# Optimization experiments

Measured on AMD Instinct MI355X. Metric: run time of the kernel, lower is better.

The kernel has to match this reference:

```python
import jax, jax.numpy as jnp
import numpy as np

SIGMA = 1.0
RADIUS = int(4.0 * SIGMA + 0.5)  # scipy/skimage truncate=4.0

_t = np.arange(-RADIUS, RADIUS + 1, dtype=np.float32)
_w = np.exp(-0.5 * (_t / SIGMA) ** 2)
KERNEL = jnp.asarray(_w / _w.sum())  # [2*RADIUS+1]


def _blur_axis(x, axis):
    """1D Gaussian filter along `axis` with 'nearest' (edge) boundary."""
    pads = [(0, 0)] * x.ndim
    pads[axis] = (RADIUS, RADIUS)
    xp = jnp.pad(x, pads, mode='edge')
    n = x.shape[axis]
    out = KERNEL[0] * jax.lax.slice_in_dim(xp, 0, n, axis=axis)
    for k in range(1, 2 * RADIUS + 1):
        out = out + KERNEL[k] * jax.lax.slice_in_dim(xp, k, k + n, axis=axis)
    return out


def gaussian_blur(x):
    # skimage.filters.gaussian on each [T, F] sample: blur over both axes
    x = _blur_axis(x, axis=1)  # time axis
    x = _blur_axis(x, axis=2)  # feature axis
    return x


def lstm_last_hidden(x, W_ih, W_hh, b_ih, b_hh):
    B, T, F = x.shape
    H = W_hh.shape[1]
    # precompute input projections for all timesteps: [B, T, 4H]
    xg = jnp.einsum('btf,gf->btg', x, W_ih) + b_ih + b_hh
    xg = jnp.transpose(xg, (1, 0, 2))  # [T, B, 4H]

    def step(carry, xt):
        h, c = carry
        g = xt + h @ W_hh.T  # [B, 4H]
        i, f, gg, o = jnp.split(g, 4, axis=-1)  # torch gate order i,f,g,o
        i = jax.nn.sigmoid(i)
        f = jax.nn.sigmoid(f)
        gg = jnp.tanh(gg)
        o = jax.nn.sigmoid(o)
        c = f * c + i * gg
        h = o * jnp.tanh(c)
        return (h, c), None

    h0 = jnp.zeros((B, H), dtype=x.dtype)
    c0 = jnp.zeros((B, H), dtype=x.dtype)
    (h_last, _), _ = jax.lax.scan(step, (h0, c0), xg)
    return h_last  # [B, H]


def setup_inputs() -> dict:
    key = jax.random.key(0)
    ks = jax.random.split(key, 7)
    B, T, F, H, O = 64, 1024, 256, 1024, 256
    s_ih = 1.0 / np.sqrt(F)
    s_hh = 1.0 / np.sqrt(H)
    return {
        'x': jax.random.uniform(ks[0], (B, T, F), dtype=jnp.float32),
        'W_ih': jax.random.normal(ks[1], (4 * H, F), dtype=jnp.float32) * s_ih,
        'W_hh': jax.random.normal(ks[2], (4 * H, H), dtype=jnp.float32) * s_hh,
        'b_ih': jax.random.normal(ks[3], (4 * H,), dtype=jnp.float32) * s_hh,
        'b_hh': jax.random.normal(ks[4], (4 * H,), dtype=jnp.float32) * s_hh,
        'W_fc': jax.random.normal(ks[5], (O, H), dtype=jnp.float32) * s_hh,
        'b_fc': jax.random.normal(ks[6], (O,), dtype=jnp.float32) * s_hh,
    }


def reference(x, W_ih, W_hh, b_ih, b_hh, W_fc, b_fc):
    xb = gaussian_blur(x)
    h_last = lstm_last_hidden(xb, W_ih, W_hh, b_ih, b_hh)
    return h_last @ W_fc.T + b_fc  # [B, O]
```

## Files before the change

kernel.cpp:

```cpp
#include <hip/hip_runtime.h>

typedef __bf16 bf16x8 __attribute__((ext_vector_type(8)));
typedef float f32x4 __attribute__((ext_vector_type(4)));

#define T_STEPS 1024
#define H_SZ    1024
#define F_IN    256
#define NGROUP  4
#define NB      16
#define WPG     64

__device__ __forceinline__ unsigned short f2bf(float f) {
    union { float f; unsigned u; } v; v.f = f;
    unsigned r = v.u + 0x7fffu + ((v.u >> 16) & 1u);
    return (unsigned short)(r >> 16);
}

__device__ __forceinline__ float fsigmoid(float x) {
    return 1.0f / (1.0f + __expf(-x));
}
__device__ __forceinline__ float ftanh(float x) {
    return 1.0f - 2.0f / (__expf(2.0f * x) + 1.0f);
}

__global__ __launch_bounds__(256) void blur_kernel(
    const float* __restrict__ x, unsigned short* __restrict__ xb)
{
    __shared__ float tb[64][256];
    const float kk[9] = {
        0.000133831f, 0.0044318617f, 0.0539911273f, 0.2419714457f,
        0.3989434694f,
        0.2419714457f, 0.0539911273f, 0.0044318617f, 0.000133831f };

    const int b     = blockIdx.x >> 4;
    const int chunk = blockIdx.x & 15;
    const int t0    = chunk * 64;
    const int f     = threadIdx.x;
    const float* xbase = x + (size_t)b * T_STEPS * F_IN;

    for (int r = 0; r < 64; r++) {
        int t = t0 + r;
        float acc = 0.0f;
        #pragma unroll
        for (int d = 0; d < 9; d++) {
            int ts = t + d - 4;
            ts = min(max(ts, 0), T_STEPS - 1);
            acc += kk[d] * xbase[ts * F_IN + f];
        }
        tb[r][f] = acc;
    }
    __syncthreads();
    for (int r = 0; r < 64; r++) {
        float acc = 0.0f;
        #pragma unroll
        for (int d = 0; d < 9; d++) {
            int fs = f + d - 4;
            fs = min(max(fs, 0), F_IN - 1);
            acc += kk[d] * tb[r][fs];
        }
        xb[((size_t)b * T_STEPS + t0 + r) * F_IN + f] = f2bf(acc);
    }
}

__global__ __launch_bounds__(256, 1) void lstm_persist(
    const unsigned short* __restrict__ xb,
    const float* __restrict__ Whh,
    const float* __restrict__ Wih,
    const float* __restrict__ bih,
    const float* __restrict__ bhh,
    unsigned short* __restrict__ hbuf,
    unsigned int* __restrict__ arrive)
{
    const int wg   = blockIdx.x;
    const int grp  = wg >> 6;
    const int w    = wg & 63;
    const int tid  = threadIdx.x;
    const int q    = tid >> 6;
    const int lane = tid & 63;
    const int lrow = lane & 15;
    const int lq   = lane >> 4;

    __shared__ f32x4 part[4][4][64];

    bf16x8 wa[8][4];
    bf16x8 wx[2][4];
    const int row_lo = w * 16 + lrow;
    #pragma unroll
    for (int kt = 0; kt < 8; kt++) {
        const int kofs = q * 256 + kt * 32 + lq * 8;
        #pragma unroll
        for (int g = 0; g < 4; g++) {
            const float* src = Whh + (size_t)(g * H_SZ + row_lo) * H_SZ + kofs;
            union { bf16x8 v; unsigned short s[8]; } u;
            #pragma unroll
            for (int j = 0; j < 8; j++) u.s[j] = f2bf(src[j]);
            wa[kt][g] = u.v;
        }
    }
    #pragma unroll
    for (int kt = 0; kt < 2; kt++) {
        const int kofs = q * 64 + kt * 32 + lq * 8;
        #pragma unroll
        for (int g = 0; g < 4; g++) {
            const float* src = Wih + (size_t)(g * H_SZ + row_lo) * F_IN + kofs;
            union { bf16x8 v; unsigned short s[8]; } u;
            #pragma unroll
            for (int j = 0; j < 8; j++) u.s[j] = f2bf(src[j]);
            wx[kt][g] = u.v;
        }
    }

    const int uhid = tid & 15;
    const int ub   = tid >> 4;
    float bias[4];
    #pragma unroll
    for (int g = 0; g < 4; g++) {
        int r = g * H_SZ + w * 16 + uhid;
        bias[g] = bih[r] + bhh[r];
    }
    float c_reg = 0.0f;

    const int b_abs_l = grp * NB + lrow;
    const unsigned short* xrow_base =
        xb + ((size_t)b_abs_l * T_STEPS) * F_IN + q * 64 + lq * 8;
    unsigned short* hdst =
        hbuf + (size_t)(grp * NB + ub) * H_SZ + w * 16 + uhid;

    for (int t = 0; t < T_STEPS; t++) {
        const unsigned short* xrow = xrow_base + (size_t)t * F_IN;
        bf16x8 xf0 = *reinterpret_cast<const bf16x8*>(xrow);
        bf16x8 xf1 = *reinterpret_cast<const bf16x8*>(xrow + 32);

        const unsigned short* hprev =
            hbuf + ((size_t)((t & 1) ^ 1) * 64 + b_abs_l) * H_SZ
                 + q * 256 + lq * 8;
        bf16x8 hf0, hf1, hf2, hf3, hf4, hf5, hf6, hf7;
        asm volatile(
            "global_load_dwordx4 %0, %8, off sc0 sc1\n\t"
            "global_load_dwordx4 %1, %8, off offset:64 sc0 sc1\n\t"
            "global_load_dwordx4 %2, %8, off offset:128 sc0 sc1\n\t"
            "global_load_dwordx4 %3, %8, off offset:192 sc0 sc1\n\t"
            "global_load_dwordx4 %4, %8, off offset:256 sc0 sc1\n\t"
            "global_load_dwordx4 %5, %8, off offset:320 sc0 sc1\n\t"
            "global_load_dwordx4 %6, %8, off offset:384 sc0 sc1\n\t"
            "global_load_dwordx4 %7, %8, off offset:448 sc0 sc1\n\t"
            "s_waitcnt vmcnt(0)"
            : "=&v"(hf0), "=&v"(hf1), "=&v"(hf2), "=&v"(hf3),
              "=&v"(hf4), "=&v"(hf5), "=&v"(hf6), "=&v"(hf7)
            : "v"(hprev)
            : "memory");
        bf16x8 hfa[8] = { hf0, hf1, hf2, hf3, hf4, hf5, hf6, hf7 };

        f32x4 acc[4];
        #pragma unroll
        for (int g = 0; g < 4; g++) acc[g] = (f32x4){0.f, 0.f, 0.f, 0.f};
        #pragma unroll
        for (int kt = 0; kt < 8; kt++)
            #pragma unroll
            for (int g = 0; g < 4; g++)
                acc[g] = __builtin_amdgcn_mfma_f32_16x16x32_bf16(
                    wa[kt][g], hfa[kt], acc[g], 0, 0, 0);
        acc[0] = __builtin_amdgcn_mfma_f32_16x16x32_bf16(wx[0][0], xf0, acc[0], 0, 0, 0);
        acc[1] = __builtin_amdgcn_mfma_f32_16x16x32_bf16(wx[0][1], xf0, acc[1], 0, 0, 0);
        acc[2] = __builtin_amdgcn_mfma_f32_16x16x32_bf16(wx[0][2], xf0, acc[2], 0, 0, 0);
        acc[3] = __builtin_amdgcn_mfma_f32_16x16x32_bf16(wx[0][3], xf0, acc[3], 0, 0, 0);
        acc[0] = __builtin_amdgcn_mfma_f32_16x16x32_bf16(wx[1][0], xf1, acc[0], 0, 0, 0);
        acc[1] = __builtin_amdgcn_mfma_f32_16x16x32_bf16(wx[1][1], xf1, acc[1], 0, 0, 0);
        acc[2] = __builtin_amdgcn_mfma_f32_16x16x32_bf16(wx[1][2], xf1, acc[2], 0, 0, 0);
        acc[3] = __builtin_amdgcn_mfma_f32_16x16x32_bf16(wx[1][3], xf1, acc[3], 0, 0, 0);

        #pragma unroll
        for (int g = 0; g < 4; g++)
            part[q][g][lane] = acc[g];
        __syncthreads();

        float gv[4];
        #pragma unroll
        for (int g = 0; g < 4; g++) {
            float s = bias[g];
            #pragma unroll
            for (int qq = 0; qq < 4; qq++)
                s += part[qq][g][(uhid >> 2) * 16 + ub][uhid & 3];
            gv[g] = s;
        }
        float ig = fsigmoid(gv[0]);
        float fg = fsigmoid(gv[1]);
        float gg = ftanh(gv[2]);
        float og = fsigmoid(gv[3]);
        c_reg = fg * c_reg + ig * gg;
        float hv = og * ftanh(c_reg);

        unsigned short hb = f2bf(hv);
        unsigned short* dst = hdst + (size_t)(t & 1) * 64 * H_SZ;
        asm volatile(
            "global_store_short %0, %1, off sc0 sc1\n\t"
            "s_waitcnt vmcnt(0)"
            :: "v"(dst), "v"(hb)
            : "memory");
        __syncthreads();

        if (tid == 0) {
            unsigned int* ctr = &arrive[grp * T_STEPS + t];
            __hip_atomic_fetch_add(ctr, 1u, __ATOMIC_RELAXED,
                                   __HIP_MEMORY_SCOPE_AGENT);
            while (__hip_atomic_load(ctr, __ATOMIC_RELAXED,
                                     __HIP_MEMORY_SCOPE_AGENT) < (unsigned)WPG) {}
        }
        __syncthreads();
    }
}

__global__ __launch_bounds__(256) void final_fc(
    const unsigned short* __restrict__ hbuf,
    const float* __restrict__ Wfc, const float* __restrict__ bfc,
    float* __restrict__ out)
{
    __shared__ float hs[H_SZ];
    const int b = blockIdx.x;
    const unsigned short* hrow = hbuf + (size_t)64 * H_SZ + (size_t)b * H_SZ;
    for (int k = threadIdx.x; k < H_SZ; k += 256) {
        union { unsigned u; float f; } cv;
        cv.u = ((unsigned)hrow[k]) << 16;
        hs[k] = cv.f;
    }
    __syncthreads();
    const int o = threadIdx.x;
    const float4* wr = reinterpret_cast<const float4*>(Wfc + (size_t)o * H_SZ);
    float acc = bfc[o];
    for (int k4 = 0; k4 < H_SZ / 4; k4++) {
        float4 wv = wr[k4];
        acc += hs[k4 * 4 + 0] * wv.x + hs[k4 * 4 + 1] * wv.y
             + hs[k4 * 4 + 2] * wv.z + hs[k4 * 4 + 3] * wv.w;
    }
    out[(size_t)b * 256 + o] = acc;
}

extern "C" void kernel_launch(void* const* d_in, const int* in_sizes, int n_in,
                              void* d_out, int out_size, void* d_ws,
                              size_t ws_size, hipStream_t stream)
{
    (void)in_sizes; (void)n_in; (void)out_size; (void)ws_size;
    const float* x   = (const float*)d_in[0];
    const float* Wih = (const float*)d_in[1];
    const float* Whh = (const float*)d_in[2];
    const float* bih = (const float*)d_in[3];
    const float* bhh = (const float*)d_in[4];
    const float* Wfc = (const float*)d_in[5];
    const float* bfc = (const float*)d_in[6];
    float* out = (float*)d_out;

    char* ws = (char*)d_ws;
    unsigned short* xblur = (unsigned short*)ws;
    unsigned short* hbuf  = (unsigned short*)(ws + 33554432);
    unsigned int*   arrv  = (unsigned int*)(ws + 33554432 + 262144);

    hipMemsetAsync(hbuf, 0, 262144 + 16384, stream);

    blur_kernel<<<dim3(1024), dim3(256), 0, stream>>>(x, xblur);

    void* kargs[] = { (void*)&xblur, (void*)&Whh, (void*)&Wih,
                      (void*)&bih, (void*)&bhh, (void*)&hbuf, (void*)&arrv };
    hipLaunchCooperativeKernel((void*)lstm_persist, dim3(256), dim3(256),
                               kargs, 0, stream);

    final_fc<<<dim3(64), dim3(256), 0, stream>>>(hbuf, Wfc, bfc, out);
}
```

Measured before the change: 4.169 ms.

## Replace per-step atomic barrier with timestep-tagged hidden-state words and polling

Each hidden value is now stored as a 32-bit word with the step index in the upper half. Consumers poll their slice of the previous hidden state until every tag matches, then unpack the bf16 halves with perm instructions. This removes the per-step atomic counter, the spin barrier, the store wait and two __syncthreads, and double-buffers the LDS partials so one barrier per step is enough. In exchange it doubles the hidden-state read traffic and polls repeatedly. Correctness now depends on each 32-bit word being stored and loaded as a single unit.

Result: slower. 6.527 ms (+56.5%).

```diff
diff --git a/kernel.cpp b/kernel.cpp
--- a/kernel.cpp
+++ b/kernel.cpp
@@ -2,13 +2,12 @@
 
 typedef __bf16 bf16x8 __attribute__((ext_vector_type(8)));
 typedef float f32x4 __attribute__((ext_vector_type(4)));
+typedef int i32x4 __attribute__((ext_vector_type(4)));
 
 #define T_STEPS 1024
 #define H_SZ    1024
 #define F_IN    256
-#define NGROUP  4
 #define NB      16
-#define WPG     64
 
 __device__ __forceinline__ unsigned short f2bf(float f) {
     union { float f; unsigned u; } v; v.f = f;
@@ -68,8 +67,7 @@
     const float* __restrict__ Wih,
     const float* __restrict__ bih,
     const float* __restrict__ bhh,
-    unsigned short* __restrict__ hbuf,
-    unsigned int* __restrict__ arrive)
+    unsigned int* __restrict__ hbuf)
 {
     const int wg   = blockIdx.x;
     const int grp  = wg >> 6;
@@ -80,7 +78,7 @@
     const int lrow = lane & 15;
     const int lq   = lane >> 4;
 
-    __shared__ f32x4 part[4][4][64];
+    __shared__ f32x4 part[2][4][4][64];
 
     bf16x8 wa[8][4];
     bf16x8 wx[2][4];
@@ -123,7 +121,7 @@
     const int b_abs_l = grp * NB + lrow;
     const unsigned short* xrow_base =
         xb + ((size_t)b_abs_l * T_STEPS) * F_IN + q * 64 + lq * 8;
-    unsigned short* hdst =
+    unsigned int* hdst0 =
         hbuf + (size_t)(grp * NB + ub) * H_SZ + w * 16 + uhid;
 
     for (int t = 0; t < T_STEPS; t++) {
@@ -131,25 +129,65 @@
         bf16x8 xf0 = *reinterpret_cast<const bf16x8*>(xrow);
         bf16x8 xf1 = *reinterpret_cast<const bf16x8*>(xrow + 32);
 
-        const unsigned short* hprev =
-            hbuf + ((size_t)((t & 1) ^ 1) * 64 + b_abs_l) * H_SZ
+        const unsigned int* hprev =
+            hbuf + ((size_t)((t + 1) & 1) * 64 + b_abs_l) * H_SZ
                  + q * 256 + lq * 8;
-        bf16x8 hf0, hf1, hf2, hf3, hf4, hf5, hf6, hf7;
-        asm volatile(
-            "global_load_dwordx4 %0, %8, off sc0 sc1\n\t"
-            "global_load_dwordx4 %1, %8, off offset:64 sc0 sc1\n\t"
-            "global_load_dwordx4 %2, %8, off offset:128 sc0 sc1\n\t"
-            "global_load_dwordx4 %3, %8, off offset:192 sc0 sc1\n\t"
-            "global_load_dwordx4 %4, %8, off offset:256 sc0 sc1\n\t"
-            "global_load_dwordx4 %5, %8, off offset:320 sc0 sc1\n\t"
-            "global_load_dwordx4 %6, %8, off offset:384 sc0 sc1\n\t"
-            "global_load_dwordx4 %7, %8, off offset:448 sc0 sc1\n\t"
-            "s_waitcnt vmcnt(0)"
-            : "=&v"(hf0), "=&v"(hf1), "=&v"(hf2), "=&v"(hf3),
-              "=&v"(hf4), "=&v"(hf5), "=&v"(hf6), "=&v"(hf7)
-            : "v"(hprev)
-            : "memory");
-        bf16x8 hfa[8] = { hf0, hf1, hf2, hf3, hf4, hf5, hf6, hf7 };
+        const unsigned int expect = (unsigned)t;
+        i32x4 d0, d1, d2, d3, d4, d5, d6, d7;
+        i32x4 d8, d9, d10, d11, d12, d13, d14, d15;
+        for (;;) {
+            asm volatile(
+                "global_load_dwordx4 %0,  %16, off sc0 sc1\n\t"
+                "global_load_dwordx4 %1,  %16, off offset:16 sc0 sc1\n\t"
+                "global_load_dwordx4 %2,  %16, off offset:128 sc0 sc1\n\t"
+                "global_load_dwordx4 %3,  %16, off offset:144 sc0 sc1\n\t"
+                "global_load_dwordx4 %4,  %16, off offset:256 sc0 sc1\n\t"
+                "global_load_dwordx4 %5,  %16, off offset:272 sc0 sc1\n\t"
+                "global_load_dwordx4 %6,  %16, off offset:384 sc0 sc1\n\t"
+                "global_load_dwordx4 %7,  %16, off offset:400 sc0 sc1\n\t"
+                "global_load_dwordx4 %8,  %16, off offset:512 sc0 sc1\n\t"
+                "global_load_dwordx4 %9,  %16, off offset:528 sc0 sc1\n\t"
+                "global_load_dwordx4 %10, %16, off offset:640 sc0 sc1\n\t"
+                "global_load_dwordx4 %11, %16, off offset:656 sc0 sc1\n\t"
+                "global_load_dwordx4 %12, %16, off offset:768 sc0 sc1\n\t"
+                "global_load_dwordx4 %13, %16, off offset:784 sc0 sc1\n\t"
+                "global_load_dwordx4 %14, %16, off offset:896 sc0 sc1\n\t"
+                "global_load_dwordx4 %15, %16, off offset:912 sc0 sc1\n\t"
+                "s_waitcnt vmcnt(0)"
+                : "=&v"(d0), "=&v"(d1), "=&v"(d2), "=&v"(d3),
+                  "=&v"(d4), "=&v"(d5), "=&v"(d6), "=&v"(d7),
+                  "=&v"(d8), "=&v"(d9), "=&v"(d10), "=&v"(d11),
+                  "=&v"(d12), "=&v"(d13), "=&v"(d14), "=&v"(d15)
+                : "v"(hprev)
+                : "memory");
+            unsigned bad = 0u;
+            const i32x4* dv[16] = { &d0,&d1,&d2,&d3,&d4,&d5,&d6,&d7,
+                                    &d8,&d9,&d10,&d11,&d12,&d13,&d14,&d15 };
+            #pragma unroll
+            for (int i = 0; i < 16; i++)
+                #pragma unroll
+                for (int j = 0; j < 4; j++)
+                    bad |= (((unsigned)((*dv[i])[j])) >> 16) ^ expect;
+            if (__all((int)(bad == 0u))) break;
+            __builtin_amdgcn_s_sleep(1);
+        }
+
+        bf16x8 hfa[8];
+        {
+            const i32x4* dv[16] = { &d0,&d1,&d2,&d3,&d4,&d5,&d6,&d7,
+                                    &d8,&d9,&d10,&d11,&d12,&d13,&d14,&d15 };
+            #pragma unroll
+            for (int kt = 0; kt < 8; kt++) {
+                const unsigned* a = (const unsigned*)dv[2 * kt];
+                const unsigned* b = (const unsigned*)dv[2 * kt + 1];
+                union { bf16x8 v; unsigned u32[4]; } u;
+                u.u32[0] = __builtin_amdgcn_perm(a[1], a[0], 0x05040100);
+                u.u32[1] = __builtin_amdgcn_perm(a[3], a[2], 0x05040100);
+                u.u32[2] = __builtin_amdgcn_perm(b[1], b[0], 0x05040100);
+                u.u32[3] = __builtin_amdgcn_perm(b[3], b[2], 0x05040100);
+                hfa[kt] = u.v;
+            }
+        }
 
         f32x4 acc[4];
         #pragma unroll
@@ -160,18 +198,18 @@
             for (int g = 0; g < 4; g++)
                 acc[g] = __builtin_amdgcn_mfma_f32_16x16x32_bf16(
                     wa[kt][g], hfa[kt], acc[g], 0, 0, 0);
-        acc[0] = __builtin_amdgcn_mfma_f32_16x16x32_bf16(wx[0][0], xf0, acc[0], 0, 0, 0);
-        acc[1] = __builtin_amdgcn_mfma_f32_16x16x32_bf16(wx[0][1], xf0, acc[1], 0, 0, 0);
-        acc[2] = __builtin_amdgcn_mfma_f32_16x16x32_bf16(wx[0][2], xf0, acc[2], 0, 0, 0);
-        acc[3] = __builtin_amdgcn_mfma_f32_16x16x32_bf16(wx[0][3], xf0, acc[3], 0, 0, 0);
-        acc[0] = __builtin_amdgcn_mfma_f32_16x16x32_bf16(wx[1][0], xf1, acc[0], 0, 0, 0);
-        acc[1] = __builtin_amdgcn_mfma_f32_16x16x32_bf16(wx[1][1], xf1, acc[1], 0, 0, 0);
-        acc[2] = __builtin_amdgcn_mfma_f32_16x16x32_bf16(wx[1][2], xf1, acc[2], 0, 0, 0);
-        acc[3] = __builtin_amdgcn_mfma_f32_16x16x32_bf16(wx[1][3], xf1, acc[3], 0, 0, 0);
-
         #pragma unroll
         for (int g = 0; g < 4; g++)
-            part[q][g][lane] = acc[g];
+            acc[g] = __builtin_amdgcn_mfma_f32_16x16x32_bf16(
+                wx[0][g], xf0, acc[g], 0, 0, 0);
+        #pragma unroll
+        for (int g = 0; g < 4; g++)
+            acc[g] = __builtin_amdgcn_mfma_f32_16x16x32_bf16(
+                wx[1][g], xf1, acc[g], 0, 0, 0);
+
+        #pragma unroll
+        for (int g = 0; g < 4; g++)
+            part[t & 1][q][g][lane] = acc[g];
         __syncthreads();
 
         float gv[4];
@@ -180,7 +218,7 @@
             float s = bias[g];
             #pragma unroll
             for (int qq = 0; qq < 4; qq++)
-                s += part[qq][g][(uhid >> 2) * 16 + ub][uhid & 3];
+                s += part[t & 1][qq][g][(uhid >> 2) * 16 + ub][uhid & 3];
             gv[g] = s;
         }
         float ig = fsigmoid(gv[0]);
@@ -190,38 +228,35 @@
         c_reg = fg * c_reg + ig * gg;
         float hv = og * ftanh(c_reg);
 
-        unsigned short hb = f2bf(hv);
-        unsigned short* dst = hdst + (size_t)(t & 1) * 64 * H_SZ;
-        asm volatile(
-            "global_store_short %0, %1, off sc0 sc1\n\t"
-            "s_waitcnt vmcnt(0)"
-            :: "v"(dst), "v"(hb)
-            : "memory");
-        __syncthreads();
-
-        if (tid == 0) {
-            unsigned int* ctr = &arrive[grp * T_STEPS + t];
-            __hip_atomic_fetch_add(ctr, 1u, __ATOMIC_RELAXED,
-                                   __HIP_MEMORY_SCOPE_AGENT);
-            while (__hip_atomic_load(ctr, __ATOMIC_RELAXED,
-                                     __HIP_MEMORY_SCOPE_AGENT) < (unsigned)WPG) {}
-        }
-        __syncthreads();
-    }
+        unsigned int word = (((unsigned)t + 1u) << 16) | (unsigned)f2bf(hv);
+        unsigned int* dst = hdst0 + (size_t)(t & 1) * 64 * H_SZ;
+        asm volatile("global_store_dword %0, %1, off sc0 sc1"
+                     :: "v"(dst), "v"(word) : "memory");
+    }
+
+    asm volatile("s_waitcnt vmcnt(0)" ::: "memory");
 }
 
 __global__ __launch_bounds__(256) void final_fc(
-    const unsigned short* __restrict__ hbuf,
+    const unsigned int* __restrict__ hbuf,
     const float* __restrict__ Wfc, const float* __restrict__ bfc,
     float* __restrict__ out)
 {
     __shared__ float hs[H_SZ];
     const int b = blockIdx.x;
-    const unsigned short* hrow = hbuf + (size_t)64 * H_SZ + (size_t)b * H_SZ;
-    for (int k = threadIdx.x; k < H_SZ; k += 256) {
-        union { unsigned u; float f; } cv;
-        cv.u = ((unsigned)hrow[k]) << 16;
-        hs[k] = cv.f;
+    const unsigned int* hrow = hbuf + (size_t)64 * H_SZ + (size_t)b * H_SZ;
+    {
+        const unsigned int* src = hrow + threadIdx.x * 4;
+        i32x4 hv4;
+        asm volatile("global_load_dwordx4 %0, %1, off sc0 sc1\n\t"
+                     "s_waitcnt vmcnt(0)"
+                     : "=v"(hv4) : "v"(src) : "memory");
+        #pragma unroll
+        for (int j = 0; j < 4; j++) {
+            union { unsigned u; float f; } cv;
+            cv.u = (((unsigned)hv4[j]) & 0xffffu) << 16;
+            hs[threadIdx.x * 4 + j] = cv.f;
+        }
     }
     __syncthreads();
     const int o = threadIdx.x;
@@ -251,17 +286,21 @@
 
     char* ws = (char*)d_ws;
     unsigned short* xblur = (unsigned short*)ws;
-    unsigned short* hbuf  = (unsigned short*)(ws + 33554432);
-    unsigned int*   arrv  = (unsigned int*)(ws + 33554432 + 262144);
-
-    hipMemsetAsync(hbuf, 0, 262144 + 16384, stream);
+    unsigned int*   hbuf  = (unsigned int*)(ws + 33554432);
+
+    hipMemsetAsync(hbuf, 0, 524288, stream);
 
     blur_kernel<<<dim3(1024), dim3(256), 0, stream>>>(x, xblur);
 
     void* kargs[] = { (void*)&xblur, (void*)&Whh, (void*)&Wih,
-                      (void*)&bih, (void*)&bhh, (void*)&hbuf, (void*)&arrv };
-    hipLaunchCooperativeKernel((void*)lstm_persist, dim3(256), dim3(256),
-                               kargs, 0, stream);
+                      (void*)&bih, (void*)&bhh, (void*)&hbuf };
+    hipError_t ce = hipLaunchCooperativeKernel((void*)lstm_persist, dim3(256),
+                                               dim3(256), kargs, 0, stream);
+    if (ce != hipSuccess) {
+        (void)hipGetLastError();
+        lstm_persist<<<dim3(256), dim3(256), 0, stream>>>(
+            xblur, Whh, Wih, bih, bhh, hbuf);
+    }
 
     final_fc<<<dim3(64), dim3(256), 0, stream>>>(hbuf, Wfc, bfc, out);
 }
```

## Replace per-step atomic counter barrier with per-workgroup step flags polled per wave

Applied to the files above, without the earlier changes.

Each workgroup in the persistent LSTM now publishes its completed step number to its own flag slot. Every wave polls all 64 flags of its group (one per lane) with a wave-wide vote before loading the previous hidden state. This replaces the atomic-increment-and-spin done by one thread, removes a block-wide sync per step, and lets the x loads for the next step be issued before the wait. The final FC kernel also loads hidden values with one vector load per thread, and the launch falls back to a normal kernel launch if the cooperative launch fails. The trade-off is more polling traffic from every wave, and correctness now depends on the double-buffer ordering argument instead of an explicit full barrier.

After: 5.039 ms. +20.9%, slower.

```diff
diff --git a/kernel.cpp b/kernel.cpp
--- a/kernel.cpp
+++ b/kernel.cpp
@@ -2,13 +2,12 @@
 
 typedef __bf16 bf16x8 __attribute__((ext_vector_type(8)));
 typedef float f32x4 __attribute__((ext_vector_type(4)));
+typedef int i32x2 __attribute__((ext_vector_type(2)));
 
 #define T_STEPS 1024
 #define H_SZ    1024
 #define F_IN    256
-#define NGROUP  4
 #define NB      16
-#define WPG     64
 
 __device__ __forceinline__ unsigned short f2bf(float f) {
     union { float f; unsigned u; } v; v.f = f;
@@ -69,7 +68,7 @@
     const float* __restrict__ bih,
     const float* __restrict__ bhh,
     unsigned short* __restrict__ hbuf,
-    unsigned int* __restrict__ arrive)
+    unsigned int* __restrict__ flags)
 {
     const int wg   = blockIdx.x;
     const int grp  = wg >> 6;
@@ -123,16 +122,27 @@
     const int b_abs_l = grp * NB + lrow;
     const unsigned short* xrow_base =
         xb + ((size_t)b_abs_l * T_STEPS) * F_IN + q * 64 + lq * 8;
-    unsigned short* hdst =
+    unsigned short* hdst0 =
         hbuf + (size_t)(grp * NB + ub) * H_SZ + w * 16 + uhid;
+    const unsigned int* flag_rd = flags + ((size_t)grp << 10) + lane;
+    unsigned int* flag_wr = flags + ((size_t)grp << 10) + w;
 
     for (int t = 0; t < T_STEPS; t++) {
         const unsigned short* xrow = xrow_base + (size_t)t * F_IN;
         bf16x8 xf0 = *reinterpret_cast<const bf16x8*>(xrow);
         bf16x8 xf1 = *reinterpret_cast<const bf16x8*>(xrow + 32);
 
+        for (;;) {
+            unsigned fv;
+            asm volatile("global_load_dword %0, %1, off sc0 sc1\n\t"
+                         "s_waitcnt vmcnt(0)"
+                         : "=v"(fv) : "v"(flag_rd) : "memory");
+            if (__all((int)(fv >= (unsigned)t))) break;
+            __builtin_amdgcn_s_sleep(1);
+        }
+
         const unsigned short* hprev =
-            hbuf + ((size_t)((t & 1) ^ 1) * 64 + b_abs_l) * H_SZ
+            hbuf + ((size_t)((t + 1) & 1) * 64 + b_abs_l) * H_SZ
                  + q * 256 + lq * 8;
         bf16x8 hf0, hf1, hf2, hf3, hf4, hf5, hf6, hf7;
         asm volatile(
@@ -160,14 +170,14 @@
             for (int g = 0; g < 4; g++)
                 acc[g] = __builtin_amdgcn_mfma_f32_16x16x32_bf16(
                     wa[kt][g], hfa[kt], acc[g], 0, 0, 0);
-        acc[0] = __builtin_amdgcn_mfma_f32_16x16x32_bf16(wx[0][0], xf0, acc[0], 0, 0, 0);
-        acc[1] = __builtin_amdgcn_mfma_f32_16x16x32_bf16(wx[0][1], xf0, acc[1], 0, 0, 0);
-        acc[2] = __builtin_amdgcn_mfma_f32_16x16x32_bf16(wx[0][2], xf0, acc[2], 0, 0, 0);
-        acc[3] = __builtin_amdgcn_mfma_f32_16x16x32_bf16(wx[0][3], xf0, acc[3], 0, 0, 0);
-        acc[0] = __builtin_amdgcn_mfma_f32_16x16x32_bf16(wx[1][0], xf1, acc[0], 0, 0, 0);
-        acc[1] = __builtin_amdgcn_mfma_f32_16x16x32_bf16(wx[1][1], xf1, acc[1], 0, 0, 0);
-        acc[2] = __builtin_amdgcn_mfma_f32_16x16x32_bf16(wx[1][2], xf1, acc[2], 0, 0, 0);
-        acc[3] = __builtin_amdgcn_mfma_f32_16x16x32_bf16(wx[1][3], xf1, acc[3], 0, 0, 0);
+        #pragma unroll
+        for (int g = 0; g < 4; g++)
+            acc[g] = __builtin_amdgcn_mfma_f32_16x16x32_bf16(
+                wx[0][g], xf0, acc[g], 0, 0, 0);
+        #pragma unroll
+        for (int g = 0; g < 4; g++)
+            acc[g] = __builtin_amdgcn_mfma_f32_16x16x32_bf16(
+                wx[1][g], xf1, acc[g], 0, 0, 0);
 
         #pragma unroll
         for (int g = 0; g < 4; g++)
@@ -191,23 +201,19 @@
         float hv = og * ftanh(c_reg);
 
         unsigned short hb = f2bf(hv);
-        unsigned short* dst = hdst + (size_t)(t & 1) * 64 * H_SZ;
-        asm volatile(
-            "global_store_short %0, %1, off sc0 sc1\n\t"
-            "s_waitcnt vmcnt(0)"
-            :: "v"(dst), "v"(hb)
-            : "memory");
+        unsigned short* dst = hdst0 + (size_t)(t & 1) * 64 * H_SZ;
+        asm volatile("global_store_short %0, %1, off sc0 sc1\n\t"
+                     "s_waitcnt vmcnt(0)"
+                     :: "v"(dst), "v"(hb) : "memory");
         __syncthreads();
-
         if (tid == 0) {
-            unsigned int* ctr = &arrive[grp * T_STEPS + t];
-            __hip_atomic_fetch_add(ctr, 1u, __ATOMIC_RELAXED,
-                                   __HIP_MEMORY_SCOPE_AGENT);
-            while (__hip_atomic_load(ctr, __ATOMIC_RELAXED,
-                                     __HIP_MEMORY_SCOPE_AGENT) < (unsigned)WPG) {}
-        }
-        __syncthreads();
-    }
+            unsigned fw = (unsigned)t + 1u;
+            asm volatile("global_store_dword %0, %1, off sc0 sc1"
+                         :: "v"(flag_wr), "v"(fw) : "memory");
+        }
+    }
+
+    asm volatile("s_waitcnt vmcnt(0)" ::: "memory");
 }
 
 __global__ __launch_bounds__(256) void final_fc(
@@ -218,10 +224,21 @@
     __shared__ float hs[H_SZ];
     const int b = blockIdx.x;
     const unsigned short* hrow = hbuf + (size_t)64 * H_SZ + (size_t)b * H_SZ;
-    for (int k = threadIdx.x; k < H_SZ; k += 256) {
-        union { unsigned u; float f; } cv;
-        cv.u = ((unsigned)hrow[k]) << 16;
-        hs[k] = cv.f;
+    {
+        const unsigned short* src = hrow + threadIdx.x * 4;
+        i32x2 hv2;
+        asm volatile("global_load_dwordx2 %0, %1, off sc0 sc1\n\t"
+                     "s_waitcnt vmcnt(0)"
+                     : "=v"(hv2) : "v"(src) : "memory");
+        #pragma unroll
+        for (int j = 0; j < 2; j++) {
+            unsigned d = (unsigned)hv2[j];
+            union { unsigned u; float f; } lo, hi;
+            lo.u = (d & 0xffffu) << 16;
+            hi.u = d & 0xffff0000u;
+            hs[threadIdx.x * 4 + j * 2 + 0] = lo.f;
+            hs[threadIdx.x * 4 + j * 2 + 1] = hi.f;
+        }
     }
     __syncthreads();
     const int o = threadIdx.x;
@@ -252,16 +269,21 @@
     char* ws = (char*)d_ws;
     unsigned short* xblur = (unsigned short*)ws;
     unsigned short* hbuf  = (unsigned short*)(ws + 33554432);
-    unsigned int*   arrv  = (unsigned int*)(ws + 33554432 + 262144);
+    unsigned int*   flags = (unsigned int*)(ws + 33554432 + 262144);
 
     hipMemsetAsync(hbuf, 0, 262144 + 16384, stream);
 
     blur_kernel<<<dim3(1024), dim3(256), 0, stream>>>(x, xblur);
 
     void* kargs[] = { (void*)&xblur, (void*)&Whh, (void*)&Wih,
-                      (void*)&bih, (void*)&bhh, (void*)&hbuf, (void*)&arrv };
-    hipLaunchCooperativeKernel((void*)lstm_persist, dim3(256), dim3(256),
-                               kargs, 0, stream);
+                      (void*)&bih, (void*)&bhh, (void*)&hbuf, (void*)&flags };
+    hipError_t ce = hipLaunchCooperativeKernel((void*)lstm_persist, dim3(256),
+                                               dim3(256), kargs, 0, stream);
+    if (ce != hipSuccess) {
+        (void)hipGetLastError();
+        lstm_persist<<<dim3(256), dim3(256), 0, stream>>>(
+            xblur, Whh, Wih, bih, bhh, hbuf, flags);
+    }
 
     final_fc<<<dim3(64), dim3(256), 0, stream>>>(hbuf, Wfc, bfc, out);
 }
```
